# Optimization experiments

Measured on AMD Instinct MI355X. Metric: run time of the kernel, lower is better.

The kernel has to match this reference:

```python
import jax, jax.numpy as jnp
import numpy as np

B, F, O = 32, 26, 20
IN, G = 2048, 512
REL = 53
EPS = 1e-5  # BatchNorm1d default eps


def setup_inputs() -> dict:
    key = jax.random.key(0)
    ks = jax.random.split(key, 10)
    inp = {
        "region_feats": jax.random.normal(ks[0], (B, F, O, IN), jnp.float32),
        "region_masks": jnp.ones((B, F, O), jnp.float32),
        "rel_feats": jax.random.randint(ks[1], (B, F, O, O), 0, REL, jnp.int64),
        "tem_feats": jax.random.uniform(ks[2], (B, F * O, F * O), jnp.float32),
        # learned params (eval mode: dropout off, BN uses running stats)
        "rel_W": jax.random.normal(ks[3], (G, IN), jnp.float32) * (1.0 / np.sqrt(IN)),
        "rel_b": jnp.zeros((G,), jnp.float32),
        "rel_emb": jax.random.normal(ks[4], (REL, G), jnp.float32) * 0.02,
        "tem_W": jax.random.normal(ks[5], (G, IN), jnp.float32) * (1.0 / np.sqrt(IN)),
        "tem_b": jnp.zeros((G,), jnp.float32),
        "bn_w": jnp.ones((F * O,), jnp.float32),
        "bn_b": jnp.zeros((F * O,), jnp.float32),
        "bn_rm": jnp.zeros((F * O,), jnp.float32),
        "bn_rv": jnp.ones((F * O,), jnp.float32),
    }
    return inp


def reference(region_feats, region_masks, rel_feats, tem_feats,
              rel_W, rel_b, rel_emb, tem_W, tem_b,
              bn_w, bn_b, bn_rm, bn_rv):
    b, f, o, _ = region_feats.shape
    # ---- RELATIONAL FEATURE GRAPH ----
    # [B,F,O,G]
    rel_region = jnp.einsum("bfoi,gi->bfog", region_feats, rel_W) + rel_b
    # embedding lookup: [B,F,O,O,G]
    emb = rel_emb[rel_feats]
    mask = (rel_feats > 0).astype(region_feats.dtype)  # [B,F,O,O]
    msum = jnp.sum(mask, axis=3)                        # [B,F,O]
    # sum_j mask_ij * emb_ij  (masked reduction over neighbor dim)
    emb_sum = jnp.einsum("bfijg,bfij->bfig", emb, mask)
    # sum_j mask_ij * r_i == r_i * msum_i, so (emb_sum + r*msum)/msum
    rel_out = (emb_sum + rel_region * msum[..., None]) / msum[..., None]
    rel_out = rel_out.reshape(b, f * o, -1)
    # ---- TEMPORAL FEATURE GRAPH ----
    tem_region = jnp.einsum("bfoi,gi->bfog", region_feats, tem_W) + tem_b
    tem_region = tem_region.reshape(b, f * o, -1)
    tem_sum = jnp.sum(tem_feats, axis=2)                # [B, F*O]
    tem_out = jnp.matmul(tem_feats, tem_region) / tem_sum[..., None]
    # ---- OUTPUT ----
    out = jnp.concatenate([rel_out, tem_out], axis=-1)  # [B, F*O, 2G]
    out = jnp.tanh(out)
    # BatchNorm1d over channel dim 1 (eval mode, running stats)
    inv = bn_w / jnp.sqrt(bn_rv + EPS)                  # [F*O]
    out = (out - bn_rm[None, :, None]) * inv[None, :, None] + bn_b[None, :, None]
    return out
```

## Files before the change

kernel.cpp:

```cpp
#include <hip/hip_runtime.h>
#include <stdint.h>

#define BB 32
#define FO 520
#define M1 16640
#define KIN 2048
#define KA 2112
#define N1 1024
#define GG 512
#define K2P 576
#define M2 640

typedef unsigned short u16;
typedef short v8s __attribute__((ext_vector_type(8)));
typedef float v4f __attribute__((ext_vector_type(4)));

__device__ __forceinline__ u16 f2bf(float f) {
  union { float f; unsigned u; } v; v.f = f;
  unsigned r = v.u + 0x7fffu + ((v.u >> 16) & 1u);
  return (u16)(r >> 16);
}

__device__ __forceinline__ float fast_tanh(float x) {
  float cx = fminf(fmaxf(x, -15.f), 15.f);
  float e = __expf(2.f * cx);
  return (e - 1.f) / (e + 1.f);
}

__global__ void prep_kernel(const float* __restrict__ rf, const int* __restrict__ rel,
                            const float* __restrict__ relW, const float* __restrict__ temW,
                            const float* __restrict__ emb,
                            u16* __restrict__ A1, u16* __restrict__ Wc) {
  const int blk = blockIdx.x;
  const int t = threadIdx.x;
  const float* src;
  u16* orow;
  if (blk < M1) {
    src = rf + (size_t)blk * KIN;
    orow = A1 + (size_t)blk * KA;
  } else {
    const int n = blk - M1;
    src = (n < GG) ? (relW + (size_t)n * KIN) : (temW + (size_t)(n - GG) * KIN);
    orow = Wc + (size_t)n * KA;
  }
  const float4* p = (const float4*)src;
  float4 a = p[2 * t], b = p[2 * t + 1];
  v8s v;
  v[0] = (short)f2bf(a.x); v[1] = (short)f2bf(a.y);
  v[2] = (short)f2bf(a.z); v[3] = (short)f2bf(a.w);
  v[4] = (short)f2bf(b.x); v[5] = (short)f2bf(b.y);
  v[6] = (short)f2bf(b.z); v[7] = (short)f2bf(b.w);
  *(v8s*)(orow + t * 8) = v;
  if (t < 64) {
    float sval = 0.f;
    if (blk < M1) {
      const int* rp = rel + (size_t)blk * 20;
      int cnt = 0, ms = 0;
#pragma unroll
      for (int j = 0; j < 20; ++j) {
        int ix = rp[j];
        cnt += (ix == t + 1);
        ms += (ix > 0);
      }
      if (t < 52 && ms > 0) sval = (float)cnt / (float)ms;
    } else {
      const int n = blk - M1;
      if (n < GG && t < 52) sval = emb[(size_t)(t + 1) * GG + n];
    }
    orow[KIN + t] = f2bf(sval);
  }
}

__global__ void casta2_kernel(const float* __restrict__ tem, u16* __restrict__ A2,
                              float* __restrict__ tsum) {
  const int w = threadIdx.x >> 6;
  const int l = threadIdx.x & 63;
  const int row = blockIdx.x * 4 + w;
  const int b = row / M2, i = row % M2;
  u16* orow = A2 + (size_t)row * K2P;
  v8s z = {0, 0, 0, 0, 0, 0, 0, 0};
  if (i >= FO) {
    *(v8s*)(orow + l * 8) = z;
    if (l < 8) *(v8s*)(orow + (64 + l) * 8) = z;
    return;
  }
  const float* srow = tem + ((size_t)b * FO + i) * FO;
  float s = 0.f;
  {
    float4 a = *(const float4*)(srow + 8 * l);
    float4 bb = *(const float4*)(srow + 8 * l + 4);
    s += a.x + a.y + a.z + a.w + bb.x + bb.y + bb.z + bb.w;
    v8s v;
    v[0] = (short)f2bf(a.x); v[1] = (short)f2bf(a.y);
    v[2] = (short)f2bf(a.z); v[3] = (short)f2bf(a.w);
    v[4] = (short)f2bf(bb.x); v[5] = (short)f2bf(bb.y);
    v[6] = (short)f2bf(bb.z); v[7] = (short)f2bf(bb.w);
    *(v8s*)(orow + l * 8) = v;
  }
  if (l < 8) {
    if (l == 0) {
      float4 a = *(const float4*)(srow + 512);
      float4 bb = *(const float4*)(srow + 516);
      s += a.x + a.y + a.z + a.w + bb.x + bb.y + bb.z + bb.w;
      v8s v;
      v[0] = (short)f2bf(a.x); v[1] = (short)f2bf(a.y);
      v[2] = (short)f2bf(a.z); v[3] = (short)f2bf(a.w);
      v[4] = (short)f2bf(bb.x); v[5] = (short)f2bf(bb.y);
      v[6] = (short)f2bf(bb.z); v[7] = (short)f2bf(bb.w);
      *(v8s*)(orow + 512) = v;
    } else {
      *(v8s*)(orow + (64 + l) * 8) = z;
    }
  }
#pragma unroll
  for (int off = 32; off > 0; off >>= 1) s += __shfl_down(s, off);
  if (l == 0) tsum[(size_t)b * FO + i] = s;
}

__global__ __launch_bounds__(256) void gemm1_kernel(
    const u16* __restrict__ A, const u16* __restrict__ Wc,
    const float* __restrict__ rel_b, const float* __restrict__ tem_b,
    const float* __restrict__ bn_w, const float* __restrict__ bn_b,
    const float* __restrict__ bn_rm, const float* __restrict__ bn_rv,
    float* __restrict__ out, u16* __restrict__ BT) {
  __shared__ u16 smem[128 * 132];
  u16* As = smem;
  u16* Bs = smem + 128 * 64;
  const int tid = threadIdx.x;
  const int lane = tid & 63;
  const int wv = tid >> 6, wm = wv >> 1, wn = wv & 1;
  const int id = blockIdx.x;
  const int x = id & 7, s = id >> 3;
  int mt, ntile;
  if (s < 128) { mt = x * 16 + (s >> 3); ntile = s & 7; }
  else         { mt = 128 + (s - 128);   ntile = x; }
  const int m0 = mt * 128, n0 = ntile * 128;
  const int quad = lane >> 4, r16 = lane & 15;

  v4f acc[4][4];
#pragma unroll
  for (int i = 0; i < 4; ++i)
#pragma unroll
    for (int j = 0; j < 4; ++j) { v4f z = {0.f, 0.f, 0.f, 0.f}; acc[i][j] = z; }

  for (int k0 = 0; k0 < KA; k0 += 64) {
    __syncthreads();
#pragma unroll
    for (int i = 0; i < 4; ++i) {
      const int L = i * 256 + tid;
      const int r = L >> 3;
      const int c = (L & 7) ^ (r & 7);
      const u16* ga = A + (size_t)(m0 + r) * KA + k0 + c * 8;
      const u16* gb = Wc + (size_t)(n0 + r) * KA + k0 + c * 8;
      u16* la = &As[(size_t)(i * 256 + wv * 64) * 8];
      u16* lb = &Bs[(size_t)(i * 256 + wv * 64) * 8];
      __builtin_amdgcn_global_load_lds((const __attribute__((address_space(1))) void*)ga,
                                       (__attribute__((address_space(3))) void*)la, 16, 0, 0);
      __builtin_amdgcn_global_load_lds((const __attribute__((address_space(1))) void*)gb,
                                       (__attribute__((address_space(3))) void*)lb, 16, 0, 0);
    }
    __syncthreads();
#pragma unroll
    for (int ks = 0; ks < 2; ++ks) {
      v8s af[4], bf[4];
#pragma unroll
      for (int t4 = 0; t4 < 4; ++t4) {
        const int ra = wm * 64 + t4 * 16 + r16;
        const int rb = wn * 64 + t4 * 16 + r16;
        af[t4] = *(const v8s*)&As[ra * 64 + (((ks * 4 + quad) ^ (ra & 7)) * 8)];
        bf[t4] = *(const v8s*)&Bs[rb * 64 + (((ks * 4 + quad) ^ (rb & 7)) * 8)];
      }
#pragma unroll
      for (int mtt = 0; mtt < 4; ++mtt)
#pragma unroll
        for (int ntt = 0; ntt < 4; ++ntt)
          acc[mtt][ntt] = __builtin_amdgcn_mfma_f32_16x16x32_bf16(af[mtt], bf[ntt], acc[mtt][ntt], 0, 0, 0);
    }
  }

  if (n0 < GG) {
#pragma unroll
    for (int mtt = 0; mtt < 4; ++mtt) {
      const int mb = m0 + wm * 64 + mtt * 16 + quad * 4;
      const int bb = mb / FO;
      const int fo0 = mb - bb * FO;
#pragma unroll
      for (int ntt = 0; ntt < 4; ++ntt) {
        const int n = n0 + wn * 64 + ntt * 16 + r16;
        const float rbn = rel_b[n];
#pragma unroll
        for (int r = 0; r < 4; ++r) {
          const int fo = fo0 + r;
          const float inv = bn_w[fo] * rsqrtf(bn_rv[fo] + 1e-5f);
          out[(size_t)(mb + r) * N1 + n] =
              (fast_tanh(acc[mtt][ntt][r] + rbn) - bn_rm[fo]) * inv + bn_b[fo];
        }
      }
    }
  } else {
    __syncthreads();
#pragma unroll
    for (int mtt = 0; mtt < 4; ++mtt) {
      const int il = wm * 64 + mtt * 16 + quad * 4;
#pragma unroll
      for (int ntt = 0; ntt < 4; ++ntt) {
        const int gl = wn * 64 + ntt * 16 + r16;
        const float tb = tem_b[(n0 - GG) + gl];
        ushort4 w;
        w.x = f2bf(acc[mtt][ntt][0] + tb);
        w.y = f2bf(acc[mtt][ntt][1] + tb);
        w.z = f2bf(acc[mtt][ntt][2] + tb);
        w.w = f2bf(acc[mtt][ntt][3] + tb);
        *(ushort4*)&smem[gl * 132 + il] = w;
      }
    }
    __syncthreads();
    const int gl = tid >> 1, seg = tid & 1;
    const int g = (n0 - GG) + gl;
    const u16* src = &smem[gl * 132 + seg * 64];
    const int mbase = m0 + seg * 64;
#pragma unroll
    for (int ch = 0; ch < 8; ++ch) {
      const int m = mbase + ch * 8;
      const int b1 = m / FO;
      const int i1 = m - b1 * FO;
      ushort4 lo = *(const ushort4*)(src + ch * 8);
      ushort4 hi = *(const ushort4*)(src + ch * 8 + 4);
      u16* dst = BT + ((size_t)(b1 * GG + g)) * K2P + i1;
      *(ushort4*)dst = lo;
      *(ushort4*)(dst + 4) = hi;
    }
  }
}

__global__ __launch_bounds__(256) void gemm2_kernel(
    const u16* __restrict__ A2, const u16* __restrict__ BT,
    const float* __restrict__ tsum,
    const float* __restrict__ bn_w, const float* __restrict__ bn_b,
    const float* __restrict__ bn_rm, const float* __restrict__ bn_rv,
    float* __restrict__ out) {
  __shared__ u16 smem[2 * 128 * 64];
  u16* As = smem;
  u16* Bs = smem + 128 * 64;
  const int tid = threadIdx.x;
  const int lane = tid & 63;
  const int wv = tid >> 6, wm = wv >> 1, wn = wv & 1;
  const int m0 = blockIdx.x * 128;
  const int n0 = blockIdx.y * 128;
  const int b = blockIdx.z;
  const u16* Ab = A2 + (size_t)b * M2 * K2P;
  const u16* Bb = BT + (size_t)b * GG * K2P;
  const int quad = lane >> 4, r16 = lane & 15;

  v4f acc[4][4];
#pragma unroll
  for (int i = 0; i < 4; ++i)
#pragma unroll
    for (int j = 0; j < 4; ++j) { v4f z = {0.f, 0.f, 0.f, 0.f}; acc[i][j] = z; }

  for (int k0 = 0; k0 < K2P; k0 += 64) {
    __syncthreads();
#pragma unroll
    for (int i = 0; i < 4; ++i) {
      const int L = i * 256 + tid;
      const int r = L >> 3;
      const int c = (L & 7) ^ (r & 7);
      const u16* ga = Ab + (size_t)(m0 + r) * K2P + k0 + c * 8;
      const u16* gb = Bb + (size_t)(n0 + r) * K2P + k0 + c * 8;
      u16* la = &As[(size_t)(i * 256 + wv * 64) * 8];
      u16* lb = &Bs[(size_t)(i * 256 + wv * 64) * 8];
      __builtin_amdgcn_global_load_lds((const __attribute__((address_space(1))) void*)ga,
                                       (__attribute__((address_space(3))) void*)la, 16, 0, 0);
      __builtin_amdgcn_global_load_lds((const __attribute__((address_space(1))) void*)gb,
                                       (__attribute__((address_space(3))) void*)lb, 16, 0, 0);
    }
    __syncthreads();
#pragma unroll
    for (int ks = 0; ks < 2; ++ks) {
      v8s af[4], bf[4];
#pragma unroll
      for (int t4 = 0; t4 < 4; ++t4) {
        const int ra = wm * 64 + t4 * 16 + r16;
        const int rb = wn * 64 + t4 * 16 + r16;
        af[t4] = *(const v8s*)&As[ra * 64 + (((ks * 4 + quad) ^ (ra & 7)) * 8)];
        bf[t4] = *(const v8s*)&Bs[rb * 64 + (((ks * 4 + quad) ^ (rb & 7)) * 8)];
      }
#pragma unroll
      for (int mtt = 0; mtt < 4; ++mtt)
#pragma unroll
        for (int ntt = 0; ntt < 4; ++ntt)
          acc[mtt][ntt] = __builtin_amdgcn_mfma_f32_16x16x32_bf16(af[mtt], bf[ntt], acc[mtt][ntt], 0, 0, 0);
    }
  }

#pragma unroll
  for (int mtt = 0; mtt < 4; ++mtt) {
#pragma unroll
    for (int ntt = 0; ntt < 4; ++ntt) {
      const int g = n0 + wn * 64 + ntt * 16 + r16;
      const int ibase = m0 + wm * 64 + mtt * 16 + quad * 4;
#pragma unroll
      for (int r = 0; r < 4; ++r) {
        const int i = ibase + r;
        if (i < FO) {
          float v = acc[mtt][ntt][r] / tsum[(size_t)b * FO + i];
          float inv = bn_w[i] * rsqrtf(bn_rv[i] + 1e-5f);
          out[((size_t)(b * FO + i)) * N1 + GG + g] =
              (fast_tanh(v) - bn_rm[i]) * inv + bn_b[i];
        }
      }
    }
  }
}

extern "C" void kernel_launch(void* const* d_in, const int* in_sizes, int n_in,
                              void* d_out, int out_size, void* d_ws, size_t ws_size,
                              hipStream_t stream) {
  const float* region_feats = (const float*)d_in[0];
  const int* rel_feats = (const int*)d_in[2];
  const float* tem_feats = (const float*)d_in[3];
  const float* rel_W = (const float*)d_in[4];
  const float* rel_b = (const float*)d_in[5];
  const float* rel_emb = (const float*)d_in[6];
  const float* tem_W = (const float*)d_in[7];
  const float* tem_b = (const float*)d_in[8];
  const float* bn_w = (const float*)d_in[9];
  const float* bn_b = (const float*)d_in[10];
  const float* bn_rm = (const float*)d_in[11];
  const float* bn_rv = (const float*)d_in[12];
  float* out = (float*)d_out;

  char* base = (char*)d_ws;
  u16* A1 = (u16*)base;
  u16* Wc = (u16*)(base + 70287360);
  u16* A2 = (u16*)(base + 74612736);
  u16* BT = (u16*)(base + 98205696);
  float* tsum = (float*)(base + 117080064);

  prep_kernel<<<M1 + 1024, 256, 0, stream>>>(region_feats, rel_feats,
                                             rel_W, tem_W, rel_emb, A1, Wc);
  casta2_kernel<<<5120, 256, 0, stream>>>(tem_feats, A2, tsum);
  gemm1_kernel<<<1040, 256, 0, stream>>>(A1, Wc, rel_b, tem_b,
                                         bn_w, bn_b, bn_rm, bn_rv, out, BT);
  gemm2_kernel<<<dim3(5, 4, 32), 256, 0, stream>>>(A2, BT, tsum,
                                                   bn_w, bn_b, bn_rm, bn_rv, out);
}
```

Baseline: 451.5 us.

## Merge prep kernels, shrink GEMM tiles/LDS, hoist BN params, nontemporal stores

Merges the bf16 cast and tem-cast kernels into one launch. gemm1 now loops over K in steps of 32 with a smaller swizzled LDS buffer and precomputed load pointers, and writes BT through a half-at-a-time 16-byte vector transpose. gemm2 switches to 64x64 tiles to launch more blocks, and the epilogues hoist BN and tsum reciprocals and use nontemporal stores. The smaller K step adds more barriers per unit of work in exchange for higher occupancy.

```diff
diff --git a/kernel.cpp b/kernel.cpp
--- a/kernel.cpp
+++ b/kernel.cpp
@@ -27,55 +27,48 @@
   return (e - 1.f) / (e + 1.f);
 }
 
-__global__ void prep_kernel(const float* __restrict__ rf, const int* __restrict__ rel,
-                            const float* __restrict__ relW, const float* __restrict__ temW,
-                            const float* __restrict__ emb,
-                            u16* __restrict__ A1, u16* __restrict__ Wc) {
+__global__ void prep_all_kernel(const float* __restrict__ rf, const int* __restrict__ rel,
+                                const float* __restrict__ relW, const float* __restrict__ temW,
+                                const float* __restrict__ emb, const float* __restrict__ tem,
+                                u16* __restrict__ A1, u16* __restrict__ Wc,
+                                u16* __restrict__ A2, float* __restrict__ tsum) {
   const int blk = blockIdx.x;
   const int t = threadIdx.x;
-  const float* src;
-  u16* orow;
-  if (blk < M1) {
-    src = rf + (size_t)blk * KIN;
-    orow = A1 + (size_t)blk * KA;
-  } else {
-    const int n = blk - M1;
-    src = (n < GG) ? (relW + (size_t)n * KIN) : (temW + (size_t)(n - GG) * KIN);
-    orow = Wc + (size_t)n * KA;
-  }
-  const float4* p = (const float4*)src;
-  float4 a = p[2 * t], b = p[2 * t + 1];
-  v8s v;
-  v[0] = (short)f2bf(a.x); v[1] = (short)f2bf(a.y);
-  v[2] = (short)f2bf(a.z); v[3] = (short)f2bf(a.w);
-  v[4] = (short)f2bf(b.x); v[5] = (short)f2bf(b.y);
-  v[6] = (short)f2bf(b.z); v[7] = (short)f2bf(b.w);
-  *(v8s*)(orow + t * 8) = v;
-  if (t < 64) {
-    float sval = 0.f;
-    if (blk < M1) {
-      const int* rp = rel + (size_t)blk * 20;
-      int cnt = 0, ms = 0;
-#pragma unroll
-      for (int j = 0; j < 20; ++j) {
-        int ix = rp[j];
-        cnt += (ix == t + 1);
-        ms += (ix > 0);
-      }
-      if (t < 52 && ms > 0) sval = (float)cnt / (float)ms;
-    } else {
+  if (blk < M1 + 1024) {
+    const float* src;
+    u16* orow;
+    if (blk < M1) { src = rf + (size_t)blk * KIN; orow = A1 + (size_t)blk * KA; }
+    else {
       const int n = blk - M1;
-      if (n < GG && t < 52) sval = emb[(size_t)(t + 1) * GG + n];
-    }
-    orow[KIN + t] = f2bf(sval);
-  }
-}
-
-__global__ void casta2_kernel(const float* __restrict__ tem, u16* __restrict__ A2,
-                              float* __restrict__ tsum) {
-  const int w = threadIdx.x >> 6;
-  const int l = threadIdx.x & 63;
-  const int row = blockIdx.x * 4 + w;
+      src = (n < GG) ? (relW + (size_t)n * KIN) : (temW + (size_t)(n - GG) * KIN);
+      orow = Wc + (size_t)n * KA;
+    }
+    const float4* p = (const float4*)src;
+    float4 a = p[2 * t], b = p[2 * t + 1];
+    v8s v;
+    v[0] = (short)f2bf(a.x); v[1] = (short)f2bf(a.y);
+    v[2] = (short)f2bf(a.z); v[3] = (short)f2bf(a.w);
+    v[4] = (short)f2bf(b.x); v[5] = (short)f2bf(b.y);
+    v[6] = (short)f2bf(b.z); v[7] = (short)f2bf(b.w);
+    *(v8s*)(orow + t * 8) = v;
+    if (t < 64) {
+      float sval = 0.f;
+      if (blk < M1) {
+        const int* rp = rel + (size_t)blk * 20;
+        int cnt = 0, ms = 0;
+#pragma unroll
+        for (int j = 0; j < 20; ++j) { int ix = rp[j]; cnt += (ix == t + 1); ms += (ix > 0); }
+        if (t < 52 && ms > 0) sval = (float)cnt / (float)ms;
+      } else {
+        const int n = blk - M1;
+        if (n < GG && t < 52) sval = emb[(size_t)(t + 1) * GG + n];
+      }
+      orow[KIN + t] = f2bf(sval);
+    }
+    return;
+  }
+  const int w = t >> 6, l = t & 63;
+  const int row = (blk - (M1 + 1024)) * 4 + w;
   const int b = row / M2, i = row % M2;
   u16* orow = A2 + (size_t)row * K2P;
   v8s z = {0, 0, 0, 0, 0, 0, 0, 0};
@@ -123,9 +116,9 @@
     const float* __restrict__ bn_w, const float* __restrict__ bn_b,
     const float* __restrict__ bn_rm, const float* __restrict__ bn_rv,
     float* __restrict__ out, u16* __restrict__ BT) {
-  __shared__ u16 smem[128 * 132];
+  __shared__ u16 smem[8704];
   u16* As = smem;
-  u16* Bs = smem + 128 * 64;
+  u16* Bs = smem + 4096;
   const int tid = threadIdx.x;
   const int lane = tid & 63;
   const int wv = tid >> 6, wm = wv >> 1, wn = wv & 1;
@@ -137,45 +130,49 @@
   const int m0 = mt * 128, n0 = ntile * 128;
   const int quad = lane >> 4, r16 = lane & 15;
 
+  const u16* ga[2]; const u16* gb[2];
+  u16* la[2]; u16* lb[2];
+#pragma unroll
+  for (int i = 0; i < 2; ++i) {
+    const int L = i * 256 + tid;
+    const int r = L >> 2, sl = L & 3;
+    const int c = sl ^ ((r >> 1) & 3);
+    ga[i] = A + (size_t)(m0 + r) * KA + c * 8;
+    gb[i] = Wc + (size_t)(n0 + r) * KA + c * 8;
+    la[i] = &As[(size_t)(i * 256 + wv * 64) * 8];
+    lb[i] = &Bs[(size_t)(i * 256 + wv * 64) * 8];
+  }
+
   v4f acc[4][4];
 #pragma unroll
   for (int i = 0; i < 4; ++i)
 #pragma unroll
     for (int j = 0; j < 4; ++j) { v4f z = {0.f, 0.f, 0.f, 0.f}; acc[i][j] = z; }
 
-  for (int k0 = 0; k0 < KA; k0 += 64) {
-    __syncthreads();
-#pragma unroll
-    for (int i = 0; i < 4; ++i) {
-      const int L = i * 256 + tid;
-      const int r = L >> 3;
-      const int c = (L & 7) ^ (r & 7);
-      const u16* ga = A + (size_t)(m0 + r) * KA + k0 + c * 8;
-      const u16* gb = Wc + (size_t)(n0 + r) * KA + k0 + c * 8;
-      u16* la = &As[(size_t)(i * 256 + wv * 64) * 8];
-      u16* lb = &Bs[(size_t)(i * 256 + wv * 64) * 8];
-      __builtin_amdgcn_global_load_lds((const __attribute__((address_space(1))) void*)ga,
-                                       (__attribute__((address_space(3))) void*)la, 16, 0, 0);
-      __builtin_amdgcn_global_load_lds((const __attribute__((address_space(1))) void*)gb,
-                                       (__attribute__((address_space(3))) void*)lb, 16, 0, 0);
-    }
-    __syncthreads();
-#pragma unroll
-    for (int ks = 0; ks < 2; ++ks) {
-      v8s af[4], bf[4];
-#pragma unroll
-      for (int t4 = 0; t4 < 4; ++t4) {
-        const int ra = wm * 64 + t4 * 16 + r16;
-        const int rb = wn * 64 + t4 * 16 + r16;
-        af[t4] = *(const v8s*)&As[ra * 64 + (((ks * 4 + quad) ^ (ra & 7)) * 8)];
-        bf[t4] = *(const v8s*)&Bs[rb * 64 + (((ks * 4 + quad) ^ (rb & 7)) * 8)];
-      }
-#pragma unroll
-      for (int mtt = 0; mtt < 4; ++mtt)
-#pragma unroll
-        for (int ntt = 0; ntt < 4; ++ntt)
-          acc[mtt][ntt] = __builtin_amdgcn_mfma_f32_16x16x32_bf16(af[mtt], bf[ntt], acc[mtt][ntt], 0, 0, 0);
-    }
+  for (int k0 = 0; k0 < KA; k0 += 32) {
+    __syncthreads();
+#pragma unroll
+    for (int i = 0; i < 2; ++i) {
+      __builtin_amdgcn_global_load_lds((const __attribute__((address_space(1))) void*)ga[i],
+                                       (__attribute__((address_space(3))) void*)la[i], 16, 0, 0);
+      __builtin_amdgcn_global_load_lds((const __attribute__((address_space(1))) void*)gb[i],
+                                       (__attribute__((address_space(3))) void*)lb[i], 16, 0, 0);
+      ga[i] += 32; gb[i] += 32;
+    }
+    __syncthreads();
+    v8s af[4], bf[4];
+#pragma unroll
+    for (int t4 = 0; t4 < 4; ++t4) {
+      const int ra = wm * 64 + t4 * 16 + r16;
+      const int rb = wn * 64 + t4 * 16 + r16;
+      af[t4] = *(const v8s*)&As[ra * 32 + ((quad ^ ((ra >> 1) & 3)) * 8)];
+      bf[t4] = *(const v8s*)&Bs[rb * 32 + ((quad ^ ((rb >> 1) & 3)) * 8)];
+    }
+#pragma unroll
+    for (int mtt = 0; mtt < 4; ++mtt)
+#pragma unroll
+      for (int ntt = 0; ntt < 4; ++ntt)
+        acc[mtt][ntt] = __builtin_amdgcn_mfma_f32_16x16x32_bf16(af[mtt], bf[ntt], acc[mtt][ntt], 0, 0, 0);
   }
 
   if (n0 < GG) {
@@ -184,51 +181,58 @@
       const int mb = m0 + wm * 64 + mtt * 16 + quad * 4;
       const int bb = mb / FO;
       const int fo0 = mb - bb * FO;
+      float inv[4], rm[4], bofs[4];
+#pragma unroll
+      for (int r = 0; r < 4; ++r) {
+        const int fo = fo0 + r;
+        inv[r] = bn_w[fo] * rsqrtf(bn_rv[fo] + 1e-5f);
+        rm[r] = bn_rm[fo]; bofs[r] = bn_b[fo];
+      }
 #pragma unroll
       for (int ntt = 0; ntt < 4; ++ntt) {
         const int n = n0 + wn * 64 + ntt * 16 + r16;
         const float rbn = rel_b[n];
 #pragma unroll
         for (int r = 0; r < 4; ++r) {
-          const int fo = fo0 + r;
-          const float inv = bn_w[fo] * rsqrtf(bn_rv[fo] + 1e-5f);
-          out[(size_t)(mb + r) * N1 + n] =
-              (fast_tanh(acc[mtt][ntt][r] + rbn) - bn_rm[fo]) * inv + bn_b[fo];
+          float val = (fast_tanh(acc[mtt][ntt][r] + rbn) - rm[r]) * inv[r] + bofs[r];
+          __builtin_nontemporal_store(val, out + (size_t)(mb + r) * N1 + n);
         }
       }
     }
   } else {
     __syncthreads();
 #pragma unroll
-    for (int mtt = 0; mtt < 4; ++mtt) {
-      const int il = wm * 64 + mtt * 16 + quad * 4;
-#pragma unroll
-      for (int ntt = 0; ntt < 4; ++ntt) {
-        const int gl = wn * 64 + ntt * 16 + r16;
-        const float tb = tem_b[(n0 - GG) + gl];
-        ushort4 w;
-        w.x = f2bf(acc[mtt][ntt][0] + tb);
-        w.y = f2bf(acc[mtt][ntt][1] + tb);
-        w.z = f2bf(acc[mtt][ntt][2] + tb);
-        w.w = f2bf(acc[mtt][ntt][3] + tb);
-        *(ushort4*)&smem[gl * 132 + il] = w;
-      }
-    }
-    __syncthreads();
-    const int gl = tid >> 1, seg = tid & 1;
-    const int g = (n0 - GG) + gl;
-    const u16* src = &smem[gl * 132 + seg * 64];
-    const int mbase = m0 + seg * 64;
-#pragma unroll
-    for (int ch = 0; ch < 8; ++ch) {
-      const int m = mbase + ch * 8;
-      const int b1 = m / FO;
-      const int i1 = m - b1 * FO;
-      ushort4 lo = *(const ushort4*)(src + ch * 8);
-      ushort4 hi = *(const ushort4*)(src + ch * 8 + 4);
-      u16* dst = BT + ((size_t)(b1 * GG + g)) * K2P + i1;
-      *(ushort4*)dst = lo;
-      *(ushort4*)(dst + 4) = hi;
+    for (int p = 0; p < 2; ++p) {
+      if (p) __syncthreads();
+      if (wn == p) {
+#pragma unroll
+        for (int mtt = 0; mtt < 4; ++mtt) {
+          const int il = wm * 64 + mtt * 16 + quad * 4;
+#pragma unroll
+          for (int ntt = 0; ntt < 4; ++ntt) {
+            const int gl = ntt * 16 + r16;
+            const float tb = tem_b[(n0 - GG) + p * 64 + gl];
+            ushort4 w;
+            w.x = f2bf(acc[mtt][ntt][0] + tb);
+            w.y = f2bf(acc[mtt][ntt][1] + tb);
+            w.z = f2bf(acc[mtt][ntt][2] + tb);
+            w.w = f2bf(acc[mtt][ntt][3] + tb);
+            *(ushort4*)&smem[gl * 136 + il] = w;
+          }
+        }
+      }
+      __syncthreads();
+#pragma unroll
+      for (int pass = 0; pass < 4; ++pass) {
+        const int gl = pass * 16 + (tid >> 4);
+        const int ch = tid & 15;
+        const int m = m0 + ch * 8;
+        const int b1 = m / FO;
+        const int i1 = m - b1 * FO;
+        v8s val = *(const v8s*)&smem[gl * 136 + ch * 8];
+        const int g = (n0 - GG) + p * 64 + gl;
+        *(v8s*)(BT + ((size_t)(b1 * GG + g)) * K2P + i1) = val;
+      }
     }
   }
 }
@@ -239,74 +243,86 @@
     const float* __restrict__ bn_w, const float* __restrict__ bn_b,
     const float* __restrict__ bn_rm, const float* __restrict__ bn_rv,
     float* __restrict__ out) {
-  __shared__ u16 smem[2 * 128 * 64];
+  __shared__ u16 smem[2 * 64 * 64];
   u16* As = smem;
-  u16* Bs = smem + 128 * 64;
+  u16* Bs = smem + 4096;
   const int tid = threadIdx.x;
   const int lane = tid & 63;
   const int wv = tid >> 6, wm = wv >> 1, wn = wv & 1;
-  const int m0 = blockIdx.x * 128;
-  const int n0 = blockIdx.y * 128;
+  const int m0 = blockIdx.x * 64;
+  const int n0 = blockIdx.y * 64;
   const int b = blockIdx.z;
   const u16* Ab = A2 + (size_t)b * M2 * K2P;
   const u16* Bb = BT + (size_t)b * GG * K2P;
   const int quad = lane >> 4, r16 = lane & 15;
 
-  v4f acc[4][4];
-#pragma unroll
-  for (int i = 0; i < 4; ++i)
-#pragma unroll
-    for (int j = 0; j < 4; ++j) { v4f z = {0.f, 0.f, 0.f, 0.f}; acc[i][j] = z; }
+  const u16* gp[4]; u16* lp[4];
+#pragma unroll
+  for (int i = 0; i < 4; ++i) {
+    const int L = i * 256 + tid;
+    const int tile = L >> 9;
+    const int idx = L & 511;
+    const int r = idx >> 3, sl = idx & 7;
+    const int c = sl ^ (r & 7);
+    gp[i] = (tile ? (Bb + (size_t)(n0 + r) * K2P) : (Ab + (size_t)(m0 + r) * K2P)) + c * 8;
+    lp[i] = (tile ? Bs : As) + (size_t)((i & 1) * 256 + wv * 64) * 8;
+  }
+
+  v4f acc[2][2];
+#pragma unroll
+  for (int i = 0; i < 2; ++i)
+#pragma unroll
+    for (int j = 0; j < 2; ++j) { v4f z = {0.f, 0.f, 0.f, 0.f}; acc[i][j] = z; }
 
   for (int k0 = 0; k0 < K2P; k0 += 64) {
     __syncthreads();
 #pragma unroll
     for (int i = 0; i < 4; ++i) {
-      const int L = i * 256 + tid;
-      const int r = L >> 3;
-      const int c = (L & 7) ^ (r & 7);
-      const u16* ga = Ab + (size_t)(m0 + r) * K2P + k0 + c * 8;
-      const u16* gb = Bb + (size_t)(n0 + r) * K2P + k0 + c * 8;
-      u16* la = &As[(size_t)(i * 256 + wv * 64) * 8];
-      u16* lb = &Bs[(size_t)(i * 256 + wv * 64) * 8];
-      __builtin_amdgcn_global_load_lds((const __attribute__((address_space(1))) void*)ga,
-                                       (__attribute__((address_space(3))) void*)la, 16, 0, 0);
-      __builtin_amdgcn_global_load_lds((const __attribute__((address_space(1))) void*)gb,
-                                       (__attribute__((address_space(3))) void*)lb, 16, 0, 0);
+      __builtin_amdgcn_global_load_lds((const __attribute__((address_space(1))) void*)gp[i],
+                                       (__attribute__((address_space(3))) void*)lp[i], 16, 0, 0);
+      gp[i] += 64;
     }
     __syncthreads();
 #pragma unroll
     for (int ks = 0; ks < 2; ++ks) {
-      v8s af[4], bf[4];
-#pragma unroll
-      for (int t4 = 0; t4 < 4; ++t4) {
-        const int ra = wm * 64 + t4 * 16 + r16;
-        const int rb = wn * 64 + t4 * 16 + r16;
+      v8s af[2], bf[2];
+#pragma unroll
+      for (int t4 = 0; t4 < 2; ++t4) {
+        const int ra = wm * 32 + t4 * 16 + r16;
+        const int rb = wn * 32 + t4 * 16 + r16;
         af[t4] = *(const v8s*)&As[ra * 64 + (((ks * 4 + quad) ^ (ra & 7)) * 8)];
         bf[t4] = *(const v8s*)&Bs[rb * 64 + (((ks * 4 + quad) ^ (rb & 7)) * 8)];
       }
 #pragma unroll
-      for (int mtt = 0; mtt < 4; ++mtt)
-#pragma unroll
-        for (int ntt = 0; ntt < 4; ++ntt)
+      for (int mtt = 0; mtt < 2; ++mtt)
+#pragma unroll
+        for (int ntt = 0; ntt < 2; ++ntt)
           acc[mtt][ntt] = __builtin_amdgcn_mfma_f32_16x16x32_bf16(af[mtt], bf[ntt], acc[mtt][ntt], 0, 0, 0);
     }
   }
 
 #pragma unroll
-  for (int mtt = 0; mtt < 4; ++mtt) {
-#pragma unroll
-    for (int ntt = 0; ntt < 4; ++ntt) {
-      const int g = n0 + wn * 64 + ntt * 16 + r16;
-      const int ibase = m0 + wm * 64 + mtt * 16 + quad * 4;
+  for (int mtt = 0; mtt < 2; ++mtt) {
+    const int ibase = m0 + wm * 32 + mtt * 16 + quad * 4;
+    float ts[4], inv[4], rm[4], bofs[4];
+#pragma unroll
+    for (int r = 0; r < 4; ++r) {
+      const int i = ibase + r;
+      if (i < FO) {
+        ts[r] = 1.f / tsum[(size_t)b * FO + i];
+        inv[r] = bn_w[i] * rsqrtf(bn_rv[i] + 1e-5f);
+        rm[r] = bn_rm[i]; bofs[r] = bn_b[i];
+      }
+    }
+#pragma unroll
+    for (int ntt = 0; ntt < 2; ++ntt) {
+      const int g = n0 + wn * 32 + ntt * 16 + r16;
 #pragma unroll
       for (int r = 0; r < 4; ++r) {
         const int i = ibase + r;
         if (i < FO) {
-          float v = acc[mtt][ntt][r] / tsum[(size_t)b * FO + i];
-          float inv = bn_w[i] * rsqrtf(bn_rv[i] + 1e-5f);
-          out[((size_t)(b * FO + i)) * N1 + GG + g] =
-              (fast_tanh(v) - bn_rm[i]) * inv + bn_b[i];
+          float val = (fast_tanh(acc[mtt][ntt][r] * ts[r]) - rm[r]) * inv[r] + bofs[r];
+          __builtin_nontemporal_store(val, out + ((size_t)(b * FO + i)) * N1 + GG + g);
         }
       }
     }
@@ -337,11 +353,10 @@
   u16* BT = (u16*)(base + 98205696);
   float* tsum = (float*)(base + 117080064);
 
-  prep_kernel<<<M1 + 1024, 256, 0, stream>>>(region_feats, rel_feats,
-                                             rel_W, tem_W, rel_emb, A1, Wc);
-  casta2_kernel<<<5120, 256, 0, stream>>>(tem_feats, A2, tsum);
+  prep_all_kernel<<<M1 + 1024 + 5120, 256, 0, stream>>>(
+      region_feats, rel_feats, rel_W, tem_W, rel_emb, tem_feats, A1, Wc, A2, tsum);
   gemm1_kernel<<<1040, 256, 0, stream>>>(A1, Wc, rel_b, tem_b,
                                          bn_w, bn_b, bn_rm, bn_rv, out, BT);
-  gemm2_kernel<<<dim3(5, 4, 32), 256, 0, stream>>>(A2, BT, tsum,
-                                                   bn_w, bn_b, bn_rm, bn_rv, out);
-}
+  gemm2_kernel<<<dim3(10, 8, 32), 256, 0, stream>>>(A2, BT, tsum,
+                                                    bn_w, bn_b, bn_rm, bn_rv, out);
+}
```

New measurement: 442.8 us. No clear change (-1.9%).
